# Kernel optimization log

Hardware: AMD Instinct MI355X
Metric: run time of the kernel (lower is better)

## Reference

```python
import jax, jax.numpy as jnp
import numpy as np

D_MODEL = 1024
NUM_HEADS = 16
HEAD_DIM = D_MODEL // NUM_HEADS


def setup_inputs() -> dict:
    key = jax.random.key(0)
    ks = jax.random.split(key, 9)
    B, T = 2, 2048
    s = 1.0 / np.sqrt(D_MODEL)
    return {
        "x": jax.random.normal(ks[0], (B, T, D_MODEL), dtype=jnp.float32),
        "Wq": jax.random.normal(ks[1], (D_MODEL, D_MODEL), dtype=jnp.float32) * s,
        "bq": jnp.zeros((D_MODEL,), dtype=jnp.float32),
        "Wk": jax.random.normal(ks[2], (D_MODEL, D_MODEL), dtype=jnp.float32) * s,
        "bk": jnp.zeros((D_MODEL,), dtype=jnp.float32),
        "Wv": jax.random.normal(ks[3], (D_MODEL, D_MODEL), dtype=jnp.float32) * s,
        "bv": jnp.zeros((D_MODEL,), dtype=jnp.float32),
        "Wo": jax.random.normal(ks[4], (D_MODEL, D_MODEL), dtype=jnp.float32) * s,
        "bo": jnp.zeros((D_MODEL,), dtype=jnp.float32),
    }


def reference(x, Wq, bq, Wk, bk, Wv, bv, Wo, bo):
    B, T, D = x.shape
    H, Hd = NUM_HEADS, HEAD_DIM
    # Linear projections; weights stored as [in, out] (torch Linear transposed)
    q = (x @ Wq + bq).reshape(B, T, H, Hd)
    k = (x @ Wk + bk).reshape(B, T, H, Hd)
    v = (x @ Wv + bv).reshape(B, T, H, Hd)
    scale = 1.0 / jnp.sqrt(jnp.asarray(Hd, dtype=x.dtype))
    scores = jnp.einsum("bqhd,bkhd->bhqk", q, k) * scale  # [B,H,T,T]
    attn = jax.nn.softmax(scores, axis=-1)
    ctx = jnp.einsum("bhqk,bkhd->bqhd", attn, v).reshape(B, T, D)
    return ctx @ Wo + bo
```

## Files before the change

### kernel.cpp

```cpp
#include <hip/hip_runtime.h>


typedef unsigned short ushort_t;
typedef __attribute__((ext_vector_type(8))) short bf16x8;
typedef __attribute__((ext_vector_type(4))) short bf16x4;
typedef __attribute__((ext_vector_type(4))) float f32x4;

#define BATCH 2
#define SEQ   2048
#define DM    1024
#define NH    16
#define HD    64
#define MTOT  (BATCH*SEQ)

__device__ __forceinline__ ushort_t f2bf(float f) {
    union { float f; unsigned int u; } v; v.f = f;
    unsigned int r = v.u + 0x7fffu + ((v.u >> 16) & 1u);
    return (ushort_t)(r >> 16);
}

__device__ __forceinline__ void gload_lds16(const void* g, void* l) {
    __builtin_amdgcn_global_load_lds(
        (const __attribute__((address_space(1))) unsigned int*)g,
        (__attribute__((address_space(3))) unsigned int*)l, 16, 0, 0);
}

__global__ __launch_bounds__(256) void packx_kernel(const float* __restrict__ x,
                                                    ushort_t* __restrict__ xb) {
    int i = blockIdx.x * 256 + threadIdx.x;
    float4 v = ((const float4*)x)[i];
    ushort4 o;
    o.x = f2bf(v.x); o.y = f2bf(v.y); o.z = f2bf(v.z); o.w = f2bf(v.w);
    ((ushort4*)xb)[i] = o;
}

__global__ __launch_bounds__(256) void wt_kernel(const float* __restrict__ W0,
                                                 const float* __restrict__ W1,
                                                 const float* __restrict__ W2,
                                                 const float* __restrict__ W3,
                                                 ushort_t* __restrict__ Wtb) {
    const float* Ws[4] = {W0, W1, W2, W3};
    const float* W = Ws[blockIdx.z];
    ushort_t* Wt = Wtb + (size_t)blockIdx.z * DM * DM;
    __shared__ ushort_t tile[64][72];
    int k0 = blockIdx.y * 64, n0 = blockIdx.x * 64;
    int tid = threadIdx.x;
    int tr = tid >> 4;
    int tc = (tid & 15) * 4;
#pragma unroll
    for (int j = 0; j < 4; j++) {
        int r = j * 16 + tr;
        float4 v = *(const float4*)&W[(size_t)(k0 + r) * DM + n0 + tc];
        tile[r][tc + 0] = f2bf(v.x); tile[r][tc + 1] = f2bf(v.y);
        tile[r][tc + 2] = f2bf(v.z); tile[r][tc + 3] = f2bf(v.w);
    }
    __syncthreads();
#pragma unroll
    for (int j = 0; j < 4; j++) {
        int n = j * 16 + tr;
        ushort4 o;
        o.x = tile[tc + 0][n]; o.y = tile[tc + 1][n];
        o.z = tile[tc + 2][n]; o.w = tile[tc + 3][n];
        *(ushort4*)&Wt[(size_t)(n0 + n) * DM + k0 + tc] = o;
    }
}

__global__ __launch_bounds__(256) void gemm_qkv(const ushort_t* __restrict__ A,
                                                const ushort_t* __restrict__ Wtb,
                                                const float* __restrict__ bq,
                                                const float* __restrict__ bk,
                                                const float* __restrict__ bv,
                                                ushort_t* __restrict__ qo,
                                                ushort_t* __restrict__ ko,
                                                ushort_t* __restrict__ vo) {
    __shared__ ushort_t As[128 * 32];
    __shared__ ushort_t Bs[128 * 32];
    int sel = blockIdx.x >> 3;
    const ushort_t* Wt = Wtb + (size_t)sel * DM * DM;
    const float* bias = sel == 0 ? bq : (sel == 1 ? bk : bv);
    int tid = threadIdx.x;
    int w = tid >> 6, lane = tid & 63, lr = lane & 15, lg = lane >> 4;
    int wr = w >> 1, wc = w & 1;
    int m0 = blockIdx.y * 128, n0 = (blockIdx.x & 7) * 128;

    f32x4 acc[4][4] = {};

    for (int k0 = 0; k0 < DM; k0 += 32) {
#pragma unroll
        for (int p = 0; p < 2; p++) {
            int c = w * 2 + p;
            int row = c * 16 + (lane >> 2);
            int cb = (lane & 3) * 8;
            gload_lds16(&A[(size_t)(m0 + row) * DM + k0 + cb], (char*)As + c * 1024);
            gload_lds16(&Wt[(size_t)(n0 + row) * DM + k0 + cb], (char*)Bs + c * 1024);
        }
        __syncthreads();
        bf16x8 af[4], bfr[4];
#pragma unroll
        for (int i = 0; i < 4; i++) {
            af[i]  = *(const bf16x8*)&As[(wr * 64 + i * 16 + lr) * 32 + lg * 8];
            bfr[i] = *(const bf16x8*)&Bs[(wc * 64 + i * 16 + lr) * 32 + lg * 8];
        }
#pragma unroll
        for (int mi = 0; mi < 4; mi++)
#pragma unroll
            for (int ni = 0; ni < 4; ni++)
                acc[mi][ni] = __builtin_amdgcn_mfma_f32_16x16x32_bf16(
                    af[mi], bfr[ni], acc[mi][ni], 0, 0, 0);
        __syncthreads();
    }

    float scale = (sel == 0) ? 0.125f : 1.0f;
#pragma unroll
    for (int mi = 0; mi < 4; mi++) {
#pragma unroll
        for (int ni = 0; ni < 4; ni++) {
            f32x4 a = acc[mi][ni];
            int n = n0 + wc * 64 + ni * 16 + lr;
            float bs = bias[n];
            int mbase = m0 + wr * 64 + mi * 16 + lg * 4;
            int hh = n >> 6, d = n & 63;
            if (sel == 2) {
                int b = mbase >> 11, tt = mbase & 2047;
                size_t base = ((size_t)(b * NH + hh) * HD + d) * SEQ + tt;
                ushort4 pk;
                pk.x = f2bf(a[0] + bs); pk.y = f2bf(a[1] + bs);
                pk.z = f2bf(a[2] + bs); pk.w = f2bf(a[3] + bs);
                *(ushort4*)&vo[base] = pk;
            } else {
                ushort_t* o = sel ? ko : qo;
#pragma unroll
                for (int r = 0; r < 4; r++) {
                    int m = mbase + r;
                    int b = m >> 11, tt = m & 2047;
                    o[((size_t)(b * NH + hh) * SEQ + tt) * HD + d] =
                        f2bf((a[r] + bs) * scale);
                }
            }
        }
    }
}

__global__ __launch_bounds__(256) void gemm_out(const ushort_t* __restrict__ A,
                                                const ushort_t* __restrict__ Wt,
                                                const float* __restrict__ bias,
                                                float* __restrict__ out) {
    __shared__ ushort_t As[128 * 32];
    __shared__ ushort_t Bs[128 * 32];
    int tid = threadIdx.x;
    int w = tid >> 6, lane = tid & 63, lr = lane & 15, lg = lane >> 4;
    int wr = w >> 1, wc = w & 1;
    int m0 = blockIdx.y * 128, n0 = blockIdx.x * 128;

    f32x4 acc[4][4] = {};

    for (int k0 = 0; k0 < DM; k0 += 32) {
#pragma unroll
        for (int p = 0; p < 2; p++) {
            int c = w * 2 + p;
            int row = c * 16 + (lane >> 2);
            int cb = (lane & 3) * 8;
            gload_lds16(&A[(size_t)(m0 + row) * DM + k0 + cb], (char*)As + c * 1024);
            gload_lds16(&Wt[(size_t)(n0 + row) * DM + k0 + cb], (char*)Bs + c * 1024);
        }
        __syncthreads();
        bf16x8 af[4], bfr[4];
#pragma unroll
        for (int i = 0; i < 4; i++) {
            af[i]  = *(const bf16x8*)&As[(wr * 64 + i * 16 + lr) * 32 + lg * 8];
            bfr[i] = *(const bf16x8*)&Bs[(wc * 64 + i * 16 + lr) * 32 + lg * 8];
        }
#pragma unroll
        for (int mi = 0; mi < 4; mi++)
#pragma unroll
            for (int ni = 0; ni < 4; ni++)
                acc[mi][ni] = __builtin_amdgcn_mfma_f32_16x16x32_bf16(
                    af[mi], bfr[ni], acc[mi][ni], 0, 0, 0);
        __syncthreads();
    }

#pragma unroll
    for (int mi = 0; mi < 4; mi++) {
#pragma unroll
        for (int ni = 0; ni < 4; ni++) {
            f32x4 a = acc[mi][ni];
            int n = n0 + wc * 64 + ni * 16 + lr;
            float bs = bias[n];
            int mbase = m0 + wr * 64 + mi * 16 + lg * 4;
#pragma unroll
            for (int r = 0; r < 4; r++)
                out[(size_t)(mbase + r) * DM + n] = a[r] + bs;
        }
    }
}

__global__ __launch_bounds__(512, 4) void attn_kernel(const ushort_t* __restrict__ Q,
                                                      const ushort_t* __restrict__ Kb,
                                                      const ushort_t* __restrict__ Vt,
                                                      ushort_t* __restrict__ Ctx) {
    __shared__ ushort_t Ks[128 * 64];
    __shared__ ushort_t Vs[64 * 128];

    int tid = threadIdx.x, w = tid >> 6, lane = tid & 63, lr = lane & 15, lg = lane >> 4;
    int orig = blockIdx.x;
    int wg = (orig & 7) * 64 + (orig >> 3);
    int qb = wg & 15, bh = wg >> 4;
    int q0 = qb * 128;

    const ushort_t* Qp = Q + (size_t)bh * SEQ * HD;
    const ushort_t* Kp = Kb + (size_t)bh * SEQ * HD;
    const ushort_t* Vp = Vt + (size_t)bh * HD * SEQ;

    int qrow = q0 + w * 16 + lr;
    bf16x8 aq[2];
    aq[0] = *(const bf16x8*)&Qp[(size_t)qrow * HD + lg * 8];
    aq[1] = *(const bf16x8*)&Qp[(size_t)qrow * HD + 32 + lg * 8];

    f32x4 oacc[4] = {};
    float m_run = -1e30f, l_run = 0.f;

    int krow = tid >> 3, kch = tid & 7;
    int kbyte = krow * 128 + ((kch * 16) ^ ((krow & 7) << 4));
    const ushort_t* kg0 = &Kp[(size_t)krow * HD + kch * 8];
    const ushort_t* kg1 = &Kp[(size_t)(krow + 64) * HD + kch * 8];
    int vrow = tid >> 4, vch = tid & 15;
    int S_a2 = (((vch >> 1) & 3) * 32 + (vch & 1) * 16 + (vch >> 3) * 4) * 2;
    int vswz = (vrow & 7) << 4;
    int vbyte0 = vrow * 256 + (S_a2 ^ vswz);
    int vbyte1 = vrow * 256 + ((S_a2 + 16) ^ vswz);
    const ushort_t* vg0 = &Vp[(size_t)vrow * SEQ + vch * 8];
    const ushort_t* vg1 = &Vp[(size_t)(vrow + 32) * SEQ + vch * 8];

    bf16x8 kr0 = *(const bf16x8*)kg0;
    bf16x8 kr1 = *(const bf16x8*)kg1;
    bf16x8 vr0 = *(const bf16x8*)vg0;
    bf16x8 vr1 = *(const bf16x8*)vg1;

    int kread = lr * 128;
    int kswz = (lr & 7) << 4;

    for (int t = 0; t < SEQ / 128; ++t) {
        if (t) __syncthreads();
        *(bf16x8*)((char*)Ks + kbyte) = kr0;
        *(bf16x8*)((char*)Ks + kbyte + 64 * 128) = kr1;
        union { bf16x8 v; bf16x4 h[2]; } u0, u1;
        u0.v = vr0; u1.v = vr1;
        *(bf16x4*)((char*)Vs + vbyte0) = u0.h[0];
        *(bf16x4*)((char*)Vs + vbyte1) = u0.h[1];
        *(bf16x4*)((char*)Vs + vbyte0 + 32 * 256) = u1.h[0];
        *(bf16x4*)((char*)Vs + vbyte1 + 32 * 256) = u1.h[1];
        __syncthreads();

        if (t + 1 < SEQ / 128) {
            size_t ko_off = (size_t)(t + 1) * 128 * HD;
            int vo_off = (t + 1) * 128;
            kr0 = *(const bf16x8*)(kg0 + ko_off);
            kr1 = *(const bf16x8*)(kg1 + ko_off);
            vr0 = *(const bf16x8*)(vg0 + vo_off);
            vr1 = *(const bf16x8*)(vg1 + vo_off);
        }

        f32x4 s[8];
        __builtin_amdgcn_s_setprio(1);
#pragma unroll
        for (int nt = 0; nt < 8; ++nt) {
            f32x4 a = {};
#pragma unroll
            for (int kk = 0; kk < 2; ++kk) {
                bf16x8 bk = *(const bf16x8*)((char*)Ks + nt * 2048 + kread +
                                             ((kk * 64 + lg * 16) ^ kswz));
                a = __builtin_amdgcn_mfma_f32_16x16x32_bf16(bk, aq[kk], a, 0, 0, 0);
            }
            s[nt] = a;
        }
        __builtin_amdgcn_s_setprio(0);

        float vmax = s[0][0];
#pragma unroll
        for (int nt = 0; nt < 8; ++nt)
#pragma unroll
            for (int r = 0; r < 4; ++r) vmax = fmaxf(vmax, s[nt][r]);
        vmax = fmaxf(vmax, __shfl_xor(vmax, 16));
        vmax = fmaxf(vmax, __shfl_xor(vmax, 32));
        float newm = fmaxf(m_run, vmax);
        float corr = __expf(m_run - newm);
        m_run = newm;
        float rs = 0.f;
#pragma unroll
        for (int nt = 0; nt < 8; ++nt)
#pragma unroll
            for (int r = 0; r < 4; ++r) {
                float p = __expf(s[nt][r] - newm);
                s[nt][r] = p;
                rs += p;
            }
        rs += __shfl_xor(rs, 16);
        rs += __shfl_xor(rs, 32);
        l_run = l_run * corr + rs;
        float cr[4];
#pragma unroll
        for (int r = 0; r < 4; ++r) cr[r] = __shfl(corr, lg * 4 + r);
#pragma unroll
        for (int dt = 0; dt < 4; ++dt)
#pragma unroll
            for (int r = 0; r < 4; ++r) oacc[dt][r] *= cr[r];

        int4 pwv[4];
#pragma unroll
        for (int kk = 0; kk < 4; ++kk) {
            unsigned pw[4];
#pragma unroll
            for (int hh = 0; hh < 2; ++hh)
#pragma unroll
                for (int pr = 0; pr < 2; ++pr) {
                    union { float f; unsigned u; } pl, ph;
                    pl.f = s[kk + 4 * hh][2 * pr];
                    ph.f = s[kk + 4 * hh][2 * pr + 1];
                    pw[hh * 2 + pr] = __builtin_amdgcn_perm(
                        ph.u + 0x8000u, pl.u + 0x8000u, 0x07060302u);
                }
            pwv[kk] = make_int4(pw[0], pw[1], pw[2], pw[3]);
        }

        __builtin_amdgcn_s_setprio(1);
#pragma unroll
        for (int dt = 0; dt < 4; ++dt) {
            int vbase = (dt * 16 + lr) * 256;
#pragma unroll
            for (int kk = 0; kk < 4; ++kk) {
                bf16x8 bv = *(const bf16x8*)((char*)Vs + vbase +
                                             ((kk * 64 + lg * 16) ^ kswz));
                oacc[dt] = __builtin_amdgcn_mfma_f32_16x16x32_bf16(
                    *(bf16x8*)&pwv[kk], bv, oacc[dt], 0, 0, 0);
            }
        }
        __builtin_amdgcn_s_setprio(0);
    }

    float inv = 1.0f / l_run;
    float iv[4];
#pragma unroll
    for (int r = 0; r < 4; ++r) iv[r] = __shfl(inv, lg * 4 + r);
    int b = bh >> 4, h = bh & 15;
#pragma unroll
    for (int dt = 0; dt < 4; ++dt)
#pragma unroll
        for (int r = 0; r < 4; ++r) {
            int q = q0 + w * 16 + lg * 4 + r;
            Ctx[((size_t)(b * SEQ + q)) * DM + h * HD + dt * 16 + lr] =
                f2bf(oacc[dt][r] * iv[r]);
        }
}

extern "C" void kernel_launch(void* const* d_in, const int* in_sizes, int n_in,
                              void* d_out, int out_size, void* d_ws, size_t ws_size,
                              hipStream_t stream) {
    const float* x  = (const float*)d_in[0];
    const float* Wq = (const float*)d_in[1];
    const float* bq = (const float*)d_in[2];
    const float* Wk = (const float*)d_in[3];
    const float* bk = (const float*)d_in[4];
    const float* Wv = (const float*)d_in[5];
    const float* bv = (const float*)d_in[6];
    const float* Wo = (const float*)d_in[7];
    const float* bo = (const float*)d_in[8];
    float* out = (float*)d_out;

    ushort_t* xbf = (ushort_t*)d_ws;
    ushort_t* wtb = xbf + (size_t)MTOT * DM;
    ushort_t* qbf = wtb + (size_t)4 * DM * DM;
    ushort_t* kbf = qbf + (size_t)MTOT * DM;
    ushort_t* vtb = kbf + (size_t)MTOT * DM;
    ushort_t* ctx = vtb + (size_t)MTOT * DM;

    packx_kernel<<<MTOT * DM / 4 / 256, 256, 0, stream>>>(x, xbf);
    wt_kernel<<<dim3(16, 16, 4), 256, 0, stream>>>(Wq, Wk, Wv, Wo, wtb);

    gemm_qkv<<<dim3(24, 32), 256, 0, stream>>>(xbf, wtb, bq, bk, bv, qbf, kbf, vtb);

    attn_kernel<<<512, 512, 0, stream>>>(qbf, kbf, vtb, ctx);

    gemm_out<<<dim3(8, 32), 256, 0, stream>>>(ctx, wtb + (size_t)3 * DM * DM, bo, out);
}
```

Measured before the change: 140.6 us.

## Double-buffer GEMM and attention LDS tiles, use exp2 with lazy softmax rescale

Adds double-buffered shared memory to the QKV and output GEMMs and the attention kernel so the next tile's loads overlap compute, with one barrier per iteration. Folds log2(e) into the Q scale so softmax uses exp2, and skips the running-max correction unless the max grows beyond a threshold. Replaces the manual bf16 packing with a packed convert instruction. It doubles LDS use, which may lower occupancy in attention, and the async LDS loads rely on barrier ordering.

```diff
diff --git a/kernel.cpp b/kernel.cpp
--- a/kernel.cpp
+++ b/kernel.cpp
@@ -12,6 +12,12 @@
 #define NH    16
 #define HD    64
 #define MTOT  (BATCH*SEQ)
+
+#if __has_builtin(__builtin_amdgcn_exp2f)
+#define EXP2(x) __builtin_amdgcn_exp2f(x)
+#else
+#define EXP2(x) exp2f(x)
+#endif
 
 __device__ __forceinline__ ushort_t f2bf(float f) {
     union { float f; unsigned int u; } v; v.f = f;
@@ -73,8 +79,8 @@
                                                 ushort_t* __restrict__ qo,
                                                 ushort_t* __restrict__ ko,
                                                 ushort_t* __restrict__ vo) {
-    __shared__ ushort_t As[128 * 32];
-    __shared__ ushort_t Bs[128 * 32];
+    __shared__ ushort_t As[2][128 * 32];
+    __shared__ ushort_t Bs[2][128 * 32];
     int sel = blockIdx.x >> 3;
     const ushort_t* Wt = Wtb + (size_t)sel * DM * DM;
     const float* bias = sel == 0 ? bq : (sel == 1 ? bk : bv);
@@ -83,23 +89,36 @@
     int wr = w >> 1, wc = w & 1;
     int m0 = blockIdx.y * 128, n0 = (blockIdx.x & 7) * 128;
 
+    int srow = (w * 2) * 16 + (lane >> 2);
+    int scb = (lane & 3) * 8;
+    const ushort_t* ag = &A[(size_t)(m0 + srow) * DM + scb];
+    const ushort_t* bg = &Wt[(size_t)(n0 + srow) * DM + scb];
+    int ldst = (w * 2) * 1024;
+
     f32x4 acc[4][4] = {};
 
-    for (int k0 = 0; k0 < DM; k0 += 32) {
-#pragma unroll
-        for (int p = 0; p < 2; p++) {
-            int c = w * 2 + p;
-            int row = c * 16 + (lane >> 2);
-            int cb = (lane & 3) * 8;
-            gload_lds16(&A[(size_t)(m0 + row) * DM + k0 + cb], (char*)As + c * 1024);
-            gload_lds16(&Wt[(size_t)(n0 + row) * DM + k0 + cb], (char*)Bs + c * 1024);
-        }
-        __syncthreads();
+#pragma unroll
+    for (int p = 0; p < 2; p++) {
+        gload_lds16(ag + (size_t)p * 16 * DM, (char*)As[0] + ldst + p * 1024);
+        gload_lds16(bg + (size_t)p * 16 * DM, (char*)Bs[0] + ldst + p * 1024);
+    }
+    __syncthreads();
+
+    for (int kt = 0; kt < 32; ++kt) {
+        int cur = kt & 1;
+        if (kt + 1 < 32) {
+            int k0 = (kt + 1) << 5;
+#pragma unroll
+            for (int p = 0; p < 2; p++) {
+                gload_lds16(ag + (size_t)p * 16 * DM + k0, (char*)As[cur ^ 1] + ldst + p * 1024);
+                gload_lds16(bg + (size_t)p * 16 * DM + k0, (char*)Bs[cur ^ 1] + ldst + p * 1024);
+            }
+        }
         bf16x8 af[4], bfr[4];
 #pragma unroll
         for (int i = 0; i < 4; i++) {
-            af[i]  = *(const bf16x8*)&As[(wr * 64 + i * 16 + lr) * 32 + lg * 8];
-            bfr[i] = *(const bf16x8*)&Bs[(wc * 64 + i * 16 + lr) * 32 + lg * 8];
+            af[i]  = *(const bf16x8*)&As[cur][(wr * 64 + i * 16 + lr) * 32 + lg * 8];
+            bfr[i] = *(const bf16x8*)&Bs[cur][(wc * 64 + i * 16 + lr) * 32 + lg * 8];
         }
 #pragma unroll
         for (int mi = 0; mi < 4; mi++)
@@ -110,7 +129,7 @@
         __syncthreads();
     }
 
-    float scale = (sel == 0) ? 0.125f : 1.0f;
+    float scale = (sel == 0) ? 0.125f * 1.44269504f : 1.0f;
 #pragma unroll
     for (int mi = 0; mi < 4; mi++) {
 #pragma unroll
@@ -145,30 +164,43 @@
                                                 const ushort_t* __restrict__ Wt,
                                                 const float* __restrict__ bias,
                                                 float* __restrict__ out) {
-    __shared__ ushort_t As[128 * 32];
-    __shared__ ushort_t Bs[128 * 32];
+    __shared__ ushort_t As[2][128 * 32];
+    __shared__ ushort_t Bs[2][128 * 32];
     int tid = threadIdx.x;
     int w = tid >> 6, lane = tid & 63, lr = lane & 15, lg = lane >> 4;
     int wr = w >> 1, wc = w & 1;
     int m0 = blockIdx.y * 128, n0 = blockIdx.x * 128;
 
+    int srow = (w * 2) * 16 + (lane >> 2);
+    int scb = (lane & 3) * 8;
+    const ushort_t* ag = &A[(size_t)(m0 + srow) * DM + scb];
+    const ushort_t* bg = &Wt[(size_t)(n0 + srow) * DM + scb];
+    int ldst = (w * 2) * 1024;
+
     f32x4 acc[4][4] = {};
 
-    for (int k0 = 0; k0 < DM; k0 += 32) {
-#pragma unroll
-        for (int p = 0; p < 2; p++) {
-            int c = w * 2 + p;
-            int row = c * 16 + (lane >> 2);
-            int cb = (lane & 3) * 8;
-            gload_lds16(&A[(size_t)(m0 + row) * DM + k0 + cb], (char*)As + c * 1024);
-            gload_lds16(&Wt[(size_t)(n0 + row) * DM + k0 + cb], (char*)Bs + c * 1024);
-        }
-        __syncthreads();
+#pragma unroll
+    for (int p = 0; p < 2; p++) {
+        gload_lds16(ag + (size_t)p * 16 * DM, (char*)As[0] + ldst + p * 1024);
+        gload_lds16(bg + (size_t)p * 16 * DM, (char*)Bs[0] + ldst + p * 1024);
+    }
+    __syncthreads();
+
+    for (int kt = 0; kt < 32; ++kt) {
+        int cur = kt & 1;
+        if (kt + 1 < 32) {
+            int k0 = (kt + 1) << 5;
+#pragma unroll
+            for (int p = 0; p < 2; p++) {
+                gload_lds16(ag + (size_t)p * 16 * DM + k0, (char*)As[cur ^ 1] + ldst + p * 1024);
+                gload_lds16(bg + (size_t)p * 16 * DM + k0, (char*)Bs[cur ^ 1] + ldst + p * 1024);
+            }
+        }
         bf16x8 af[4], bfr[4];
 #pragma unroll
         for (int i = 0; i < 4; i++) {
-            af[i]  = *(const bf16x8*)&As[(wr * 64 + i * 16 + lr) * 32 + lg * 8];
-            bfr[i] = *(const bf16x8*)&Bs[(wc * 64 + i * 16 + lr) * 32 + lg * 8];
+            af[i]  = *(const bf16x8*)&As[cur][(wr * 64 + i * 16 + lr) * 32 + lg * 8];
+            bfr[i] = *(const bf16x8*)&Bs[cur][(wc * 64 + i * 16 + lr) * 32 + lg * 8];
         }
 #pragma unroll
         for (int mi = 0; mi < 4; mi++)
@@ -198,8 +230,8 @@
                                                       const ushort_t* __restrict__ Kb,
                                                       const ushort_t* __restrict__ Vt,
                                                       ushort_t* __restrict__ Ctx) {
-    __shared__ ushort_t Ks[128 * 64];
-    __shared__ ushort_t Vs[64 * 128];
+    __shared__ ushort_t Ks[2][128 * 64];
+    __shared__ ushort_t Vs[2][64 * 128];
 
     int tid = threadIdx.x, w = tid >> 6, lane = tid & 63, lr = lane & 15, lg = lane >> 4;
     int orig = blockIdx.x;
@@ -217,7 +249,7 @@
     aq[1] = *(const bf16x8*)&Qp[(size_t)qrow * HD + 32 + lg * 8];
 
     f32x4 oacc[4] = {};
-    float m_run = -1e30f, l_run = 0.f;
+    float m_run = 0.f, l_run = 0.f;
 
     int krow = tid >> 3, kch = tid & 7;
     int kbyte = krow * 128 + ((kch * 16) ^ ((krow & 7) << 4));
@@ -231,27 +263,30 @@
     const ushort_t* vg0 = &Vp[(size_t)vrow * SEQ + vch * 8];
     const ushort_t* vg1 = &Vp[(size_t)(vrow + 32) * SEQ + vch * 8];
 
-    bf16x8 kr0 = *(const bf16x8*)kg0;
-    bf16x8 kr1 = *(const bf16x8*)kg1;
-    bf16x8 vr0 = *(const bf16x8*)vg0;
-    bf16x8 vr1 = *(const bf16x8*)vg1;
+    {
+        bf16x8 k0v = *(const bf16x8*)kg0;
+        bf16x8 k1v = *(const bf16x8*)kg1;
+        bf16x8 v0v = *(const bf16x8*)vg0;
+        bf16x8 v1v = *(const bf16x8*)vg1;
+        *(bf16x8*)((char*)Ks[0] + kbyte) = k0v;
+        *(bf16x8*)((char*)Ks[0] + kbyte + 64 * 128) = k1v;
+        union { bf16x8 v; bf16x4 h[2]; } u0, u1;
+        u0.v = v0v; u1.v = v1v;
+        *(bf16x4*)((char*)Vs[0] + vbyte0) = u0.h[0];
+        *(bf16x4*)((char*)Vs[0] + vbyte1) = u0.h[1];
+        *(bf16x4*)((char*)Vs[0] + vbyte0 + 32 * 256) = u1.h[0];
+        *(bf16x4*)((char*)Vs[0] + vbyte1 + 32 * 256) = u1.h[1];
+    }
+    __syncthreads();
 
     int kread = lr * 128;
     int kswz = (lr & 7) << 4;
 
     for (int t = 0; t < SEQ / 128; ++t) {
-        if (t) __syncthreads();
-        *(bf16x8*)((char*)Ks + kbyte) = kr0;
-        *(bf16x8*)((char*)Ks + kbyte + 64 * 128) = kr1;
-        union { bf16x8 v; bf16x4 h[2]; } u0, u1;
-        u0.v = vr0; u1.v = vr1;
-        *(bf16x4*)((char*)Vs + vbyte0) = u0.h[0];
-        *(bf16x4*)((char*)Vs + vbyte1) = u0.h[1];
-        *(bf16x4*)((char*)Vs + vbyte0 + 32 * 256) = u1.h[0];
-        *(bf16x4*)((char*)Vs + vbyte1 + 32 * 256) = u1.h[1];
-        __syncthreads();
-
-        if (t + 1 < SEQ / 128) {
+        int cur = t & 1;
+        bf16x8 kr0, kr1, vr0, vr1;
+        bool more = (t + 1 < SEQ / 128);
+        if (more) {
             size_t ko_off = (size_t)(t + 1) * 128 * HD;
             int vo_off = (t + 1) * 128;
             kr0 = *(const bf16x8*)(kg0 + ko_off);
@@ -267,7 +302,7 @@
             f32x4 a = {};
 #pragma unroll
             for (int kk = 0; kk < 2; ++kk) {
-                bf16x8 bk = *(const bf16x8*)((char*)Ks + nt * 2048 + kread +
+                bf16x8 bk = *(const bf16x8*)((char*)Ks[cur] + nt * 2048 + kread +
                                              ((kk * 64 + lg * 16) ^ kswz));
                 a = __builtin_amdgcn_mfma_f32_16x16x32_bf16(bk, aq[kk], a, 0, 0, 0);
             }
@@ -275,35 +310,45 @@
         }
         __builtin_amdgcn_s_setprio(0);
 
-        float vmax = s[0][0];
-#pragma unroll
-        for (int nt = 0; nt < 8; ++nt)
-#pragma unroll
-            for (int r = 0; r < 4; ++r) vmax = fmaxf(vmax, s[nt][r]);
+        float vm0 = fmaxf(s[0][0], s[1][0]), vm1 = fmaxf(s[0][1], s[1][1]);
+        float vm2 = fmaxf(s[0][2], s[1][2]), vm3 = fmaxf(s[0][3], s[1][3]);
+#pragma unroll
+        for (int nt = 2; nt < 8; nt += 2) {
+            vm0 = fmaxf(vm0, fmaxf(s[nt][0], s[nt + 1][0]));
+            vm1 = fmaxf(vm1, fmaxf(s[nt][1], s[nt + 1][1]));
+            vm2 = fmaxf(vm2, fmaxf(s[nt][2], s[nt + 1][2]));
+            vm3 = fmaxf(vm3, fmaxf(s[nt][3], s[nt + 1][3]));
+        }
+        float vmax = fmaxf(fmaxf(vm0, vm1), fmaxf(vm2, vm3));
         vmax = fmaxf(vmax, __shfl_xor(vmax, 16));
         vmax = fmaxf(vmax, __shfl_xor(vmax, 32));
-        float newm = fmaxf(m_run, vmax);
-        float corr = __expf(m_run - newm);
-        m_run = newm;
-        float rs = 0.f;
-#pragma unroll
-        for (int nt = 0; nt < 8; ++nt)
-#pragma unroll
-            for (int r = 0; r < 4; ++r) {
-                float p = __expf(s[nt][r] - newm);
-                s[nt][r] = p;
-                rs += p;
-            }
+        if (!__all(vmax <= m_run + 8.f)) {
+            float newm = fmaxf(m_run, vmax);
+            float corr = EXP2(m_run - newm);
+            m_run = newm;
+            l_run *= corr;
+            float cr[4];
+#pragma unroll
+            for (int r = 0; r < 4; ++r) cr[r] = __shfl(corr, lg * 4 + r);
+#pragma unroll
+            for (int dt = 0; dt < 4; ++dt)
+#pragma unroll
+                for (int r = 0; r < 4; ++r) oacc[dt][r] *= cr[r];
+        }
+        float rs0 = 0.f, rs1 = 0.f, rs2 = 0.f, rs3 = 0.f;
+#pragma unroll
+        for (int nt = 0; nt < 8; ++nt) {
+            float p0 = EXP2(s[nt][0] - m_run);
+            float p1 = EXP2(s[nt][1] - m_run);
+            float p2 = EXP2(s[nt][2] - m_run);
+            float p3 = EXP2(s[nt][3] - m_run);
+            s[nt][0] = p0; s[nt][1] = p1; s[nt][2] = p2; s[nt][3] = p3;
+            rs0 += p0; rs1 += p1; rs2 += p2; rs3 += p3;
+        }
+        float rs = (rs0 + rs1) + (rs2 + rs3);
         rs += __shfl_xor(rs, 16);
         rs += __shfl_xor(rs, 32);
-        l_run = l_run * corr + rs;
-        float cr[4];
-#pragma unroll
-        for (int r = 0; r < 4; ++r) cr[r] = __shfl(corr, lg * 4 + r);
-#pragma unroll
-        for (int dt = 0; dt < 4; ++dt)
-#pragma unroll
-            for (int r = 0; r < 4; ++r) oacc[dt][r] *= cr[r];
+        l_run += rs;
 
         int4 pwv[4];
 #pragma unroll
@@ -313,11 +358,11 @@
             for (int hh = 0; hh < 2; ++hh)
 #pragma unroll
                 for (int pr = 0; pr < 2; ++pr) {
-                    union { float f; unsigned u; } pl, ph;
-                    pl.f = s[kk + 4 * hh][2 * pr];
-                    ph.f = s[kk + 4 * hh][2 * pr + 1];
-                    pw[hh * 2 + pr] = __builtin_amdgcn_perm(
-                        ph.u + 0x8000u, pl.u + 0x8000u, 0x07060302u);
+                    unsigned rr;
+                    asm("v_cvt_pk_bf16_f32 %0, %1, %2"
+                        : "=v"(rr)
+                        : "v"(s[kk + 4 * hh][2 * pr]), "v"(s[kk + 4 * hh][2 * pr + 1]));
+                    pw[hh * 2 + pr] = rr;
                 }
             pwv[kk] = make_int4(pw[0], pw[1], pw[2], pw[3]);
         }
@@ -328,13 +373,27 @@
             int vbase = (dt * 16 + lr) * 256;
 #pragma unroll
             for (int kk = 0; kk < 4; ++kk) {
-                bf16x8 bv = *(const bf16x8*)((char*)Vs + vbase +
+                bf16x8 bv = *(const bf16x8*)((char*)Vs[cur] + vbase +
                                              ((kk * 64 + lg * 16) ^ kswz));
                 oacc[dt] = __builtin_amdgcn_mfma_f32_16x16x32_bf16(
                     *(bf16x8*)&pwv[kk], bv, oacc[dt], 0, 0, 0);
             }
         }
         __builtin_amdgcn_s_setprio(0);
+
+        if (more) {
+            char* kd = (char*)Ks[cur ^ 1];
+            char* vd = (char*)Vs[cur ^ 1];
+            *(bf16x8*)(kd + kbyte) = kr0;
+            *(bf16x8*)(kd + kbyte + 64 * 128) = kr1;
+            union { bf16x8 v; bf16x4 h[2]; } u0, u1;
+            u0.v = vr0; u1.v = vr1;
+            *(bf16x4*)(vd + vbyte0) = u0.h[0];
+            *(bf16x4*)(vd + vbyte1) = u0.h[1];
+            *(bf16x4*)(vd + vbyte0 + 32 * 256) = u1.h[0];
+            *(bf16x4*)(vd + vbyte1 + 32 * 256) = u1.h[1];
+            __syncthreads();
+        }
     }
 
     float inv = 1.0f / l_run;
```

Result: faster. 135.3 us (-3.8%).
